# Kernel tuning notes

Hardware: AMD Instinct MI355X
Metric: run time of the kernel (lower is better)

The kernel has to match this reference:

```python
import jax, jax.numpy as jnp
import numpy as np

B = 16384        # batch (population evaluation batch)
NUM_IN = 256     # input nodes
N = 1024         # total nodes
K = 8            # max fan-in (padded)
NN = N - NUM_IN  # non-input nodes, in topo order
NUM_OUT = 64


def setup_inputs() -> dict:
    key = jax.random.key(0)
    k0, k1, k2 = jax.random.split(key, 3)
    inputs = jax.random.normal(k0, (B, NUM_IN), dtype=jnp.float32)

    # Build a random DAG: node i (i >= NUM_IN) draws up to K predecessors from {0..i-1}.
    rng = np.random.default_rng(0)
    in_idx = np.zeros((NN, K), dtype=np.int32)
    edge_mask = np.zeros((NN, K), dtype=bool)
    for r in range(NN):
        node = NUM_IN + r
        deg = min(K, node)
        preds = rng.choice(node, size=deg, replace=False)
        in_idx[r, :deg] = preds
        edge_mask[r, :deg] = True

    edge_w = jax.random.normal(k1, (NN, K), dtype=jnp.float32) * 0.5
    bias = jax.random.normal(k2, (NN,), dtype=jnp.float32) * 0.1
    response = jnp.ones((NN,), dtype=jnp.float32)
    out_idx = jnp.arange(NUM_IN, N, dtype=jnp.int32)          # topo order of non-input nodes
    output_idx = jnp.arange(N - NUM_OUT, N, dtype=jnp.int32)  # output nodes
    return {
        "inputs": inputs, "edge_w": edge_w, "bias": bias, "response": response,
        "in_idx": jnp.asarray(in_idx), "edge_mask": jnp.asarray(edge_mask),
        "out_idx": out_idx, "output_idx": output_idx,
    }


def reference(inputs, edge_w, bias, response, in_idx, edge_mask, out_idx, output_idx):
    b = inputs.shape[0]
    num_in = inputs.shape[1]
    n = num_in + out_idx.shape[0]
    # node_vals[:, input_idx] = inputs  (input_idx == arange(num_in))
    node_vals = jnp.zeros((b, n), dtype=jnp.float32).at[:, :num_in].set(inputs)

    def step(carry, xs):
        idx_r, w_r, m_r, b_r, resp_r, o_r = xs
        # gather incoming node values [B, K], apply per-edge weight (conn gene)
        vals = carry[:, idx_r]
        s = jnp.sum(jnp.where(m_r, vals * w_r, 0.0), axis=1)  # node aggregation: sum
        y = jnp.tanh(b_r + resp_r * s)                        # node gene activation
        carry = carry.at[:, o_r].set(y)
        return carry, None

    node_vals, _ = jax.lax.scan(
        step, node_vals, (in_idx, edge_w, edge_mask, bias, response, out_idx)
    )
    return node_vals[:, output_idx]
```

## Files before the change

### kernel.cpp

```cpp
#include <hip/hip_runtime.h>
#include <stdint.h>
#include <stddef.h>

#define B_TOT   16384
#define NUM_IN  256
#define N_NODES 1024
#define NN      768
#define K       8
#define NUM_OUT 64
#define NB      64
#define MAXL    800
#define TPB     768
#define WPB     12

struct Rec {
  uint32_t p01, p23, p45, p67;
  uint32_t outPh;
  float    w[8];
  float    bias;
  uint32_t pad0, pad1;
};
static_assert(sizeof(Rec) == 64, "Rec must be 64B");

__global__ __launch_bounds__(NN)
void setup_kernel(const int* __restrict__ in_idx,
                  const float* __restrict__ edge_w,
                  const float* __restrict__ bias,
                  const float* __restrict__ response,
                  const int* __restrict__ out_idx,
                  int* __restrict__ g_nlev,
                  int* __restrict__ g_loff,
                  Rec* __restrict__ recs)
{
  __shared__ int lvl[N_NODES];
  __shared__ int hist[MAXL];
  __shared__ int cnt[MAXL];
  __shared__ int offs[MAXL + 2];
  __shared__ int changed;
  __shared__ int maxlv;

  const int t = threadIdx.x;

  for (int i = t; i < N_NODES; i += NN) lvl[i] = 0;
  for (int i = t; i < MAXL; i += NN) { hist[i] = 0; cnt[i] = 0; }
  if (t == 0) maxlv = 0;

  int idxs[K];
#pragma unroll
  for (int k = 0; k < K; ++k)
    idxs[k] = in_idx[t * K + k];
  __syncthreads();

  for (int iter = 0; iter < 800; ++iter) {
    int nl = 0;
#pragma unroll
    for (int k = 0; k < K; ++k) {
      int l = lvl[idxs[k]];
      nl = (l > nl) ? l : nl;
    }
    nl += 1;
    __syncthreads();
    if (t == 0) changed = 0;
    int cur = lvl[NUM_IN + t];
    __syncthreads();
    if (nl != cur) { lvl[NUM_IN + t] = nl; changed = 1; }
    __syncthreads();
    if (changed == 0) break;
  }

  const int L = lvl[NUM_IN + t];
  atomicAdd(&hist[L], 1);
  atomicMax(&maxlv, L);
  __syncthreads();
  const int ml = maxlv;
  if (t == 0) {
    offs[1] = 0;
    for (int l = 1; l <= ml; ++l) offs[l + 1] = offs[l] + hist[l];
  }
  __syncthreads();
  const int pos = offs[L] + atomicAdd(&cnt[L], 1);

  uint32_t P[K];
#pragma unroll
  for (int k = 0; k < K; ++k) {
    uint32_t id = (uint32_t)idxs[k];
    P[k] = id * 64u + ((id & 31u) << 1);
  }
  Rec r;
  r.p01 = P[0] | (P[1] << 16);
  r.p23 = P[2] | (P[3] << 16);
  r.p45 = P[4] | (P[5] << 16);
  r.p67 = P[6] | (P[7] << 16);
  uint32_t oid = (uint32_t)out_idx[t];
  r.outPh = oid * 64u + ((oid & 31u) << 1);
  const float rsp = response[t];
#pragma unroll
  for (int k = 0; k < K; ++k) r.w[k] = edge_w[t * K + k] * rsp;
  r.bias = bias[t];
  r.pad0 = 0; r.pad1 = 0;
  recs[pos] = r;

  if (t <= ml) g_loff[t] = offs[t + 1];
  if (t == 0)  g_nlev[0] = ml;
}

__global__ __launch_bounds__(TPB, 3)
void eval_kernel(const float* __restrict__ inputs,
                 const int* __restrict__ output_idx,
                 const int* __restrict__ g_nlev,
                 const int* __restrict__ g_loff,
                 const Rec* __restrict__ recs,
                 float* __restrict__ out)
{
  __shared__ _Float16 vals[N_NODES * NB];
  __shared__ int      loffs[MAXL + 1];

  const uint32_t tid  = threadIdx.x;
  const uint32_t lane = tid & 63u;
  const uint32_t wave = tid >> 6;
  const int      base = blockIdx.x * NB;

  const int nlev = g_nlev[0];
  for (int i = (int)tid; i <= nlev; i += TPB) loffs[i] = g_loff[i];

  const uint32_t col = tid & 255u;
  const uint32_t cg  = tid >> 8;
  const uint32_t swz = col * 64u + ((col & 31u) << 1);
  for (uint32_t c = cg; c < NB; c += 3) {
    float v = inputs[(size_t)(base + c) * NUM_IN + col];
    vals[swz ^ c] = (_Float16)v;
  }
  __syncthreads();

  for (int l = 0; l < nlev; ++l) {
    const int beg = loffs[l], end = loffs[l + 1];
    int j = beg + (int)wave;
    if (j < end) {
      Rec rr = recs[__builtin_amdgcn_readfirstlane(j)];
      for (;;) {
        const int jn = j + WPB;
        const bool has = jn < end;
        Rec rn;
        if (has) rn = recs[__builtin_amdgcn_readfirstlane(jn)];

        const uint32_t P0 = rr.p01 & 0xFFFFu, P1 = rr.p01 >> 16;
        const uint32_t P2 = rr.p23 & 0xFFFFu, P3 = rr.p23 >> 16;
        const uint32_t P4 = rr.p45 & 0xFFFFu, P5 = rr.p45 >> 16;
        const uint32_t P6 = rr.p67 & 0xFFFFu, P7 = rr.p67 >> 16;

        float v0 = (float)vals[P0 ^ lane];
        float v1 = (float)vals[P1 ^ lane];
        float v2 = (float)vals[P2 ^ lane];
        float v3 = (float)vals[P3 ^ lane];
        float v4 = (float)vals[P4 ^ lane];
        float v5 = (float)vals[P5 ^ lane];
        float v6 = (float)vals[P6 ^ lane];
        float v7 = (float)vals[P7 ^ lane];

        float s0 = __builtin_fmaf(rr.w[0], v0, rr.bias);
        float s1 = rr.w[1] * v1;
        float s2 = rr.w[2] * v2;
        float s3 = rr.w[3] * v3;
        s0 = __builtin_fmaf(rr.w[4], v4, s0);
        s1 = __builtin_fmaf(rr.w[5], v5, s1);
        s2 = __builtin_fmaf(rr.w[6], v6, s2);
        s3 = __builtin_fmaf(rr.w[7], v7, s3);
        const float x = (s0 + s1) + (s2 + s3);

        const float e  = __expf(x + x);
        const float rc = __builtin_amdgcn_rcpf(e + 1.0f);
        const float y  = __builtin_fmaf(-2.0f, rc, 1.0f);

        vals[(rr.outPh & 0xFFFFu) ^ lane] = (_Float16)y;

        if (!has) break;
        rr = rn; j = jn;
      }
    }
    __syncthreads();
  }

  const uint32_t oid  = (uint32_t)output_idx[lane];
  const uint32_t oswz = oid * 64u + ((oid & 31u) << 1);
  for (uint32_t k = 0; k < 6; ++k) {
    const uint32_t b = wave + k * 12u;
    if (b < NB) {
      float v = (float)vals[oswz ^ b];
      out[(size_t)(base + b) * NUM_OUT + lane] = v;
    }
  }
}

extern "C" void kernel_launch(void* const* d_in, const int* in_sizes, int n_in,
                              void* d_out, int out_size, void* d_ws, size_t ws_size,
                              hipStream_t stream)
{
  (void)in_sizes; (void)n_in; (void)out_size; (void)ws_size;

  const float* inputs     = (const float*)d_in[0];
  const float* edge_w     = (const float*)d_in[1];
  const float* bias       = (const float*)d_in[2];
  const float* response   = (const float*)d_in[3];
  const int*   in_idx     = (const int*)d_in[4];
  const int*   out_idx    = (const int*)d_in[6];
  const int*   output_idx = (const int*)d_in[7];
  float*       out        = (float*)d_out;

  char* ws = (char*)d_ws;
  int* g_nlev = (int*)ws;
  int* g_loff = (int*)(ws + 256);
  Rec* recs   = (Rec*)(ws + 8192);

  hipLaunchKernelGGL(setup_kernel, dim3(1), dim3(NN), 0, stream,
                     in_idx, edge_w, bias, response, out_idx,
                     g_nlev, g_loff, recs);
  hipLaunchKernelGGL(eval_kernel, dim3(B_TOT / NB), dim3(TPB), 0, stream,
                     inputs, output_idx, g_nlev, g_loff, recs, out);
}
```

Baseline: 136.1 us.

## Use fp16 dot2 for node sums and widen eval blocks to 16 waves

```diff
diff --git a/kernel.cpp b/kernel.cpp
--- a/kernel.cpp
+++ b/kernel.cpp
@@ -10,13 +10,15 @@
 #define NUM_OUT 64
 #define NB      64
 #define MAXL    800
-#define TPB     768
-#define WPB     12
+#define TPB     1024
+#define WPB     16
+
+typedef _Float16 h2 __attribute__((ext_vector_type(2)));
 
 struct Rec {
-  uint32_t p01, p23, p45, p67;
+  uint32_t p[8];
+  uint32_t w01, w23, w45, w67;
   uint32_t outPh;
-  float    w[8];
   float    bias;
   uint32_t pad0, pad1;
 };
@@ -80,22 +82,25 @@
   __syncthreads();
   const int pos = offs[L] + atomicAdd(&cnt[L], 1);
 
-  uint32_t P[K];
+  Rec r;
 #pragma unroll
   for (int k = 0; k < K; ++k) {
     uint32_t id = (uint32_t)idxs[k];
-    P[k] = id * 64u + ((id & 31u) << 1);
-  }
-  Rec r;
-  r.p01 = P[0] | (P[1] << 16);
-  r.p23 = P[2] | (P[3] << 16);
-  r.p45 = P[4] | (P[5] << 16);
-  r.p67 = P[6] | (P[7] << 16);
+    r.p[k] = id * 64u + ((id & 31u) << 1);
+  }
+  const float rsp = response[t];
+  uint16_t hw[K];
+#pragma unroll
+  for (int k = 0; k < K; ++k) {
+    _Float16 h = (_Float16)(edge_w[t * K + k] * rsp);
+    hw[k] = __builtin_bit_cast(uint16_t, h);
+  }
+  r.w01 = (uint32_t)hw[0] | ((uint32_t)hw[1] << 16);
+  r.w23 = (uint32_t)hw[2] | ((uint32_t)hw[3] << 16);
+  r.w45 = (uint32_t)hw[4] | ((uint32_t)hw[5] << 16);
+  r.w67 = (uint32_t)hw[6] | ((uint32_t)hw[7] << 16);
   uint32_t oid = (uint32_t)out_idx[t];
   r.outPh = oid * 64u + ((oid & 31u) << 1);
-  const float rsp = response[t];
-#pragma unroll
-  for (int k = 0; k < K; ++k) r.w[k] = edge_w[t * K + k] * rsp;
   r.bias = bias[t];
   r.pad0 = 0; r.pad1 = 0;
   recs[pos] = r;
@@ -104,7 +109,7 @@
   if (t == 0)  g_nlev[0] = ml;
 }
 
-__global__ __launch_bounds__(TPB, 3)
+__global__ __launch_bounds__(TPB, 4)
 void eval_kernel(const float* __restrict__ inputs,
                  const int* __restrict__ output_idx,
                  const int* __restrict__ g_nlev,
@@ -126,7 +131,7 @@
   const uint32_t col = tid & 255u;
   const uint32_t cg  = tid >> 8;
   const uint32_t swz = col * 64u + ((col & 31u) << 1);
-  for (uint32_t c = cg; c < NB; c += 3) {
+  for (uint32_t c = cg; c < NB; c += 4) {
     float v = inputs[(size_t)(base + c) * NUM_IN + col];
     vals[swz ^ c] = (_Float16)v;
   }
@@ -143,35 +148,47 @@
         Rec rn;
         if (has) rn = recs[__builtin_amdgcn_readfirstlane(jn)];
 
-        const uint32_t P0 = rr.p01 & 0xFFFFu, P1 = rr.p01 >> 16;
-        const uint32_t P2 = rr.p23 & 0xFFFFu, P3 = rr.p23 >> 16;
-        const uint32_t P4 = rr.p45 & 0xFFFFu, P5 = rr.p45 >> 16;
-        const uint32_t P6 = rr.p67 & 0xFFFFu, P7 = rr.p67 >> 16;
-
-        float v0 = (float)vals[P0 ^ lane];
-        float v1 = (float)vals[P1 ^ lane];
-        float v2 = (float)vals[P2 ^ lane];
-        float v3 = (float)vals[P3 ^ lane];
-        float v4 = (float)vals[P4 ^ lane];
-        float v5 = (float)vals[P5 ^ lane];
-        float v6 = (float)vals[P6 ^ lane];
-        float v7 = (float)vals[P7 ^ lane];
-
-        float s0 = __builtin_fmaf(rr.w[0], v0, rr.bias);
-        float s1 = rr.w[1] * v1;
-        float s2 = rr.w[2] * v2;
-        float s3 = rr.w[3] * v3;
-        s0 = __builtin_fmaf(rr.w[4], v4, s0);
-        s1 = __builtin_fmaf(rr.w[5], v5, s1);
-        s2 = __builtin_fmaf(rr.w[6], v6, s2);
-        s3 = __builtin_fmaf(rr.w[7], v7, s3);
-        const float x = (s0 + s1) + (s2 + s3);
+        const _Float16 x0 = vals[rr.p[0] ^ lane];
+        const _Float16 x1 = vals[rr.p[1] ^ lane];
+        const _Float16 x2 = vals[rr.p[2] ^ lane];
+        const _Float16 x3 = vals[rr.p[3] ^ lane];
+        const _Float16 x4 = vals[rr.p[4] ^ lane];
+        const _Float16 x5 = vals[rr.p[5] ^ lane];
+        const _Float16 x6 = vals[rr.p[6] ^ lane];
+        const _Float16 x7 = vals[rr.p[7] ^ lane];
+
+        const h2 v01 = {x0, x1};
+        const h2 v23 = {x2, x3};
+        const h2 v45 = {x4, x5};
+        const h2 v67 = {x6, x7};
+
+#if __has_builtin(__builtin_amdgcn_fdot2)
+        float x = rr.bias;
+        x = __builtin_amdgcn_fdot2(v01, __builtin_bit_cast(h2, rr.w01), x, false);
+        x = __builtin_amdgcn_fdot2(v23, __builtin_bit_cast(h2, rr.w23), x, false);
+        x = __builtin_amdgcn_fdot2(v45, __builtin_bit_cast(h2, rr.w45), x, false);
+        x = __builtin_amdgcn_fdot2(v67, __builtin_bit_cast(h2, rr.w67), x, false);
+#else
+        const h2 w01 = __builtin_bit_cast(h2, rr.w01);
+        const h2 w23 = __builtin_bit_cast(h2, rr.w23);
+        const h2 w45 = __builtin_bit_cast(h2, rr.w45);
+        const h2 w67 = __builtin_bit_cast(h2, rr.w67);
+        float s0 = __builtin_fmaf((float)w01.x, (float)v01.x, rr.bias);
+        float s1 = (float)w01.y * (float)v01.y;
+        float s2 = (float)w23.x * (float)v23.x;
+        float s3 = (float)w23.y * (float)v23.y;
+        s0 = __builtin_fmaf((float)w45.x, (float)v45.x, s0);
+        s1 = __builtin_fmaf((float)w45.y, (float)v45.y, s1);
+        s2 = __builtin_fmaf((float)w67.x, (float)v67.x, s2);
+        s3 = __builtin_fmaf((float)w67.y, (float)v67.y, s3);
+        float x = (s0 + s1) + (s2 + s3);
+#endif
 
         const float e  = __expf(x + x);
         const float rc = __builtin_amdgcn_rcpf(e + 1.0f);
         const float y  = __builtin_fmaf(-2.0f, rc, 1.0f);
 
-        vals[(rr.outPh & 0xFFFFu) ^ lane] = (_Float16)y;
+        vals[rr.outPh ^ lane] = (_Float16)y;
 
         if (!has) break;
         rr = rn; j = jn;
@@ -182,12 +199,10 @@
 
   const uint32_t oid  = (uint32_t)output_idx[lane];
   const uint32_t oswz = oid * 64u + ((oid & 31u) << 1);
-  for (uint32_t k = 0; k < 6; ++k) {
-    const uint32_t b = wave + k * 12u;
-    if (b < NB) {
-      float v = (float)vals[oswz ^ b];
-      out[(size_t)(base + b) * NUM_OUT + lane] = v;
-    }
+  for (uint32_t k = 0; k < 4; ++k) {
+    const uint32_t b = wave + k * 16u;
+    float v = (float)vals[oswz ^ b];
+    out[(size_t)(base + b) * NUM_OUT + lane] = v;
   }
 }
 
```

New measurement: 128.3 us. -5.7%, faster.
